# Performance work log

Measured on AMD Instinct MI355X. Metric: run time of the kernel, lower is better.

The kernel has to match this reference:

```python
import jax, jax.numpy as jnp
import numpy as np
import math

BS, SL, NE, NH = 4, 2048, 1024, 16
HD = NE // NH  # 64


def setup_inputs() -> dict:
    key = jax.random.key(0)
    ks = jax.random.split(key, 5)
    x = jax.random.normal(ks[0], (BS, SL, NE), dtype=jnp.float32)
    # causal mask: 1 where attending allowed (j <= i), 0 otherwise
    mask = jnp.tril(jnp.ones((SL, SL), dtype=jnp.int32))[None, None, :, :]
    s = 1.0 / math.sqrt(NE)
    Wqkv = jax.random.normal(ks[1], (NE, 3 * NE), dtype=jnp.float32) * s
    bqkv = jax.random.normal(ks[2], (3 * NE,), dtype=jnp.float32) * 0.02
    Wo = jax.random.normal(ks[3], (NE, NE), dtype=jnp.float32) * s
    bo = jax.random.normal(ks[4], (NE,), dtype=jnp.float32) * 0.02
    return {"x": x, "mask": mask, "Wqkv": Wqkv, "bqkv": bqkv, "Wo": Wo, "bo": bo}


def reference(x, mask, Wqkv, bqkv, Wo, bo):
    bs, sl, ne = x.shape
    qkv = x @ Wqkv + bqkv                       # [bs, sl, 3*ne]
    q, k, v = jnp.split(qkv, 3, axis=-1)
    # [bs, sl, ne] -> [bs, nh, sl, hd]
    q = q.reshape(bs, sl, NH, HD).transpose(0, 2, 1, 3)
    k = k.reshape(bs, sl, NH, HD).transpose(0, 2, 1, 3)
    v = v.reshape(bs, sl, NH, HD).transpose(0, 2, 1, 3)
    scale = 1.0 / math.sqrt(HD)
    att = jnp.einsum('bhqd,bhkd->bhqk', q, k) * scale  # [bs, nh, sl, sl]
    att = jnp.where(mask == 0, -jnp.inf, att)
    w = jax.nn.softmax(att, axis=-1)
    y = jnp.einsum('bhqk,bhkd->bhqd', w, v)            # [bs, nh, sl, hd]
    y = y.transpose(0, 2, 1, 3).reshape(bs, sl, ne)
    return y @ Wo + bo
```

## Files before the change

### kernel.cpp

```cpp
#include <hip/hip_runtime.h>

#define BS 4
#define SL 2048
#define NE 1024
#define NH 16
#define HD 64
#define N3 3072

typedef __attribute__((ext_vector_type(8))) __bf16 bf16x8;
typedef __attribute__((ext_vector_type(4))) float f32x4;
typedef __attribute__((ext_vector_type(4))) short s16x4;
typedef unsigned short u16;

#define CE 0.18033688011112042f

#if __has_builtin(__builtin_amdgcn_exp2f)
#define EXP2(x) __builtin_amdgcn_exp2f(x)
#else
#define EXP2(x) exp2f(x)
#endif

__device__ __forceinline__ u16 f2bf(float f) {
  union { float f; unsigned int u; } v; v.f = f;
  unsigned int r = v.u + 0x7FFFu + ((v.u >> 16) & 1u);
  return (u16)(r >> 16);
}

__device__ __forceinline__ int permpack(float a, float b) {
  return __builtin_amdgcn_perm(__float_as_uint(b), __float_as_uint(a),
                               0x07060302u);
}

__device__ __forceinline__ void gld16(const void* g, void* l) {
#if __has_builtin(__builtin_amdgcn_global_load_lds)
  __builtin_amdgcn_global_load_lds(
      (const __attribute__((address_space(1))) unsigned int*)g,
      (__attribute__((address_space(3))) unsigned int*)l, 16, 0, 0);
#else
  *(int4*)((char*)l + (size_t)(threadIdx.x & 63) * 16) = *(const int4*)g;
#endif
}

__global__ void convert_x(const float* __restrict__ x, u16* __restrict__ xb) {
  int i = (blockIdx.x * 256 + threadIdx.x) * 8;
  float4 f0 = *(const float4*)(x + i);
  float4 f1 = *(const float4*)(x + i + 4);
  union { int4 v; u16 h[8]; } p;
  p.h[0] = f2bf(f0.x); p.h[1] = f2bf(f0.y);
  p.h[2] = f2bf(f0.z); p.h[3] = f2bf(f0.w);
  p.h[4] = f2bf(f1.x); p.h[5] = f2bf(f1.y);
  p.h[6] = f2bf(f1.z); p.h[7] = f2bf(f1.w);
  *(int4*)(xb + i) = p.v;
}

__global__ void transpose_w(const float* __restrict__ W, u16* __restrict__ Wt,
                            int K, int N) {
  __shared__ u16 tile[32][33];
  int bn = blockIdx.x * 32, bk = blockIdx.y * 32;
  int tx = threadIdx.x, ty = threadIdx.y;
  for (int r = 0; r < 32; r += 8)
    tile[ty + r][tx] = f2bf(W[(size_t)(bk + ty + r) * N + bn + tx]);
  __syncthreads();
  for (int r = 0; r < 32; r += 8)
    Wt[(size_t)(bn + ty + r) * K + bk + tx] = tile[tx][ty + r];
}

#define MFMA_G(a, b, c) \
  __builtin_amdgcn_mfma_f32_16x16x32_bf16(a, b, c, 0, 0, 0)

template <int C32, int SCALEQ>
__global__ __launch_bounds__(256, 2) void gemm2b(
    const u16* __restrict__ A, const u16* __restrict__ Bt,
    const float* __restrict__ bias, void* __restrict__ C, int M, int N, int K,
    int lda) {
  constexpr int BM = 128, BN = 128, BK = 64;
  __shared__ u16 As[2][BM * BK];
  __shared__ u16 Bs[2][BN * BK];

  const int tid = threadIdx.x;
  const int w = tid >> 6, lane = tid & 63;
  const int lq = lane >> 4, lr = lane & 15;
  const int nwx = gridDim.x;
  const int nwg = nwx * gridDim.y;
  const int lin = blockIdx.y * nwx + blockIdx.x;
  const int cpx = nwg >> 3;
  const int swb = (lin & 7) * cpx + (lin >> 3);
  const int m0 = (swb / nwx) * BM, n0 = (swb % nwx) * BN;
  const int wm = (w >> 1) * 64, wn = (w & 1) * 64;

  const int l8 = lane >> 3, lb = lane & 7;
  const int sw8 = (lb ^ l8) * 8;
  const u16* gA = A + (size_t)(m0 + w * 32 + l8) * lda + sw8;
  const u16* gB = Bt + (size_t)(n0 + w * 32 + l8) * K + sw8;

#define STAGE(buf, gpa, gpb)                                  \
  do {                                                        \
    _Pragma("unroll") for (int c = 0; c < 4; c++) {           \
      gld16((gpa) + (size_t)(c * 8) * lda,                    \
            &As[buf][(w * 32 + c * 8) * 64]);                 \
      gld16((gpb) + (size_t)(c * 8) * K,                      \
            &Bs[buf][(w * 32 + c * 8) * 64]);                 \
    }                                                         \
  } while (0)

  const f32x4 fzero = {0.f, 0.f, 0.f, 0.f};
  f32x4 acc[4][4];
#pragma unroll
  for (int i = 0; i < 4; i++)
#pragma unroll
    for (int j = 0; j < 4; j++) acc[i][j] = fzero;

  const int KT = K / BK;
  STAGE(0, gA, gB);
  __syncthreads();
  const u16* gAn = gA + BK;
  const u16* gBn = gB + BK;

  for (int T = 0; T < KT; T++) {
    const int cur = T & 1;
    if (T + 1 < KT) {
      STAGE(cur ^ 1, gAn, gBn);
      gAn += BK;
      gBn += BK;
    }
    __builtin_amdgcn_sched_barrier(0);

    bf16x8 a[4][2], bfr[4][2];
#pragma unroll
    for (int i = 0; i < 4; i++)
#pragma unroll
      for (int ks = 0; ks < 2; ks++) {
        int row = wm + i * 16 + lr;
        a[i][ks] = *(const bf16x8*)
            &As[cur][row * 64 + (((ks * 4 + lq) ^ (lr & 7)) * 8)];
      }
#pragma unroll
    for (int j = 0; j < 4; j++)
#pragma unroll
      for (int ks = 0; ks < 2; ks++) {
        int row = wn + j * 16 + lr;
        bfr[j][ks] = *(const bf16x8*)
            &Bs[cur][row * 64 + (((ks * 4 + lq) ^ (lr & 7)) * 8)];
      }
    __builtin_amdgcn_s_setprio(1);
#pragma unroll
    for (int ks = 0; ks < 2; ks++)
#pragma unroll
      for (int i = 0; i < 4; i++)
#pragma unroll
        for (int j = 0; j < 4; j++)
          acc[i][j] = MFMA_G(a[i][ks], bfr[j][ks], acc[i][j]);
    __builtin_amdgcn_s_setprio(0);
    __syncthreads();
  }
#undef STAGE

#pragma unroll
  for (int j = 0; j < 4; j++) {
    int col = n0 + wn + j * 16 + lr;
    float bv = bias[col];
    float qs = (SCALEQ && col < NE) ? CE : 1.0f;
#pragma unroll
    for (int i = 0; i < 4; i++) {
#pragma unroll
      for (int r = 0; r < 4; r++) {
        int row = m0 + wm + i * 16 + lq * 4 + r;
        float val = acc[i][j][r] + bv;
        if (SCALEQ) val *= qs;
        if (C32) ((float*)C)[(size_t)row * N + col] = val;
        else     ((u16*)C)[(size_t)row * N + col]   = f2bf(val);
      }
    }
  }
}

#define KSTR 72
#define MFMA16(a, b, c) __builtin_amdgcn_mfma_f32_16x16x32_bf16(a, b, c, 0, 0, 0)
#define MFMA1616(a, b, c) \
  __builtin_amdgcn_mfma_f32_16x16x16bf16_1k(a, b, c, 0, 0, 0)

__device__ __forceinline__ void softmax_pack(f32x4 (&s)[4], s16x4 (&pa)[4],
                                             f32x4 (&o)[4], float& m_,
                                             float& l_) {
  float a0 = fmaxf(fmaxf(s[0][0], s[0][1]), s[0][2]);
  float a1 = fmaxf(fmaxf(s[0][3], s[1][0]), s[1][1]);
  float a2 = fmaxf(fmaxf(s[1][2], s[1][3]), s[2][0]);
  float a3 = fmaxf(fmaxf(s[2][1], s[2][2]), s[2][3]);
  float a4 = fmaxf(fmaxf(s[3][0], s[3][1]), s[3][2]);
  float mt = fmaxf(fmaxf(fmaxf(a0, a1), fmaxf(a2, a3)), fmaxf(a4, s[3][3]));
  mt = fmaxf(mt, __shfl_xor(mt, 16));
  mt = fmaxf(mt, __shfl_xor(mt, 32));
  bool need = !__all(mt <= m_ + 11.54f);
  float mn = need ? fmaxf(m_, mt) : m_;
  if (need) {
    float alpha = EXP2(m_ - mn);
    m_ = mn;
    l_ *= alpha;
#pragma unroll
    for (int jd = 0; jd < 4; jd++)
#pragma unroll
      for (int r = 0; r < 4; r++) o[jd][r] *= alpha;
  }
  float psum = 0.f;
#pragma unroll
  for (int j = 0; j < 4; j++) {
    float p0 = EXP2(s[j][0] - mn);
    float p1 = EXP2(s[j][1] - mn);
    float p2 = EXP2(s[j][2] - mn);
    float p3 = EXP2(s[j][3] - mn);
    psum += (p0 + p1) + (p2 + p3);
    union { int i[2]; s16x4 v; } pu;
    pu.i[0] = permpack(p0, p1);
    pu.i[1] = permpack(p2, p3);
    pa[j] = pu.v;
  }
  l_ += psum;
}

__device__ __forceinline__ void attn_step(const bf16x8& q0, const bf16x8& q1,
                                          const u16* __restrict__ Kb,
                                          const u16* __restrict__ Vb,
                                          bool diag, int qloc, int lq, int lr,
                                          f32x4 (&o)[4], float& m_, float& l_) {
  const f32x4 fzero = {0.f, 0.f, 0.f, 0.f};
  const int swz = (lq ^ ((lr >> 1) & 3)) * 8;
  f32x4 s[4];
  __builtin_amdgcn_s_setprio(1);
#pragma unroll
  for (int j = 0; j < 4; j++) {
    int kr = j * 16 + lr;
    bf16x8 kf0 = *(const bf16x8*)&Kb[kr * 32 + swz];
    bf16x8 kf1 = *(const bf16x8*)&Kb[2048 + kr * 32 + swz];
    f32x4 z = MFMA16(kf0, q0, fzero);
    s[j] = MFMA16(kf1, q1, z);
  }
  __builtin_amdgcn_s_setprio(0);
  if (diag) {
#pragma unroll
    for (int j = 0; j < 4; j++)
#pragma unroll
      for (int r = 0; r < 4; r++)
        if (16 * j + r > qloc) s[j][r] = -1e30f;
  }
  s16x4 pa[4];
  softmax_pack(s, pa, o, m_, l_);
  __builtin_amdgcn_s_setprio(1);
#pragma unroll
  for (int jd = 0; jd < 4; jd++) {
    const u16* vrow = &Vb[(jd * 16 + lr) * KSTR + lq * 16];
    union { int4 q; s16x4 h[2]; } va, vb;
    va.q = *(const int4*)vrow;
    vb.q = *(const int4*)(vrow + 8);
    o[jd] = MFMA1616(va.h[0], pa[0], o[jd]);
    o[jd] = MFMA1616(va.h[1], pa[1], o[jd]);
    o[jd] = MFMA1616(vb.h[0], pa[2], o[jd]);
    o[jd] = MFMA1616(vb.h[1], pa[3], o[jd]);
  }
  __builtin_amdgcn_s_setprio(0);
}

__global__ __launch_bounds__(256, 4) void attn_paired(u16* __restrict__ qkv) {
  __shared__ u16 Ks[2][4096];
  __shared__ u16 Vs[2][64 * KSTR];

  const int tid = threadIdx.x;
  const int w = tid >> 6, lane = tid & 63;
  const int lq = lane >> 4, lr = lane & 15;
  const int bh = blockIdx.x, p = blockIdx.y;
  const int h = bh & (NH - 1), b = bh >> 4;
  const int qt0 = p, qt1 = (SL / 64 - 1) - p;
  const int qloc = w * 16 + lr - 4 * lq;

  u16* base = qkv + (size_t)b * SL * N3;
  const u16* kbase = base + NE + h * HD;

  const int kg_key = lane >> 2;
  const int kg_blk = (lane & 3) ^ ((kg_key >> 1) & 3);
  const int skey = tid & 63, sd0 = (tid >> 6) * 8;
  const int skeyP = ((skey >> 2) & 3) * 16 + (skey >> 4) * 4 + (skey & 3);
  const u16* vrow0 = base + (size_t)skey * N3 + 2 * NE + h * HD + sd0;

#define KPRE(buf, key0)                                                     \
  {                                                                         \
    _Pragma("unroll") for (int t = 0; t < 2; t++) {                         \
      int chunk = w * 2 + t, half = chunk >> 2, kgrp = chunk & 3;           \
      const u16* g = kbase + (size_t)((key0) + kgrp * 16 + kg_key) * N3 +   \
                     half * 32 + kg_blk * 8;                                \
      gld16(g, &Ks[buf][half * 2048 + kgrp * 512]);                         \
    }                                                                       \
  }
#define VWRITE(buf)                                           \
  {                                                           \
    union { int4 v; u16 u[8]; } t0, t1;                       \
    t0.v = v0; t1.v = v1;                                     \
    u16* Vn = &Vs[buf][0];                                    \
    _Pragma("unroll") for (int j = 0; j < 8; j++) {           \
      Vn[(sd0 + j) * KSTR + skeyP] = t0.u[j];                 \
      Vn[(sd0 + 32 + j) * KSTR + skeyP] = t1.u[j];            \
    }                                                         \
  }

  bf16x8 qf[2][2];
#pragma unroll
  for (int half = 0; half < 2; half++) {
    int qt = half ? qt1 : qt0;
    const u16* qrow = base + (size_t)(qt * 64 + w * 16 + lr) * N3 + h * HD;
    qf[half][0] = *(const bf16x8*)(qrow + lq * 8);
    qf[half][1] = *(const bf16x8*)(qrow + 32 + lq * 8);
  }

  const f32x4 fzero = {0.f, 0.f, 0.f, 0.f};
  f32x4 o[2][4];
  float m_[2], l_[2];
#pragma unroll
  for (int half = 0; half < 2; half++) {
    m_[half] = -1e30f;
    l_[half] = 0.f;
#pragma unroll
    for (int jd = 0; jd < 4; jd++) o[half][jd] = fzero;
  }

  KPRE(0, 0);
  int4 v0 = *(const int4*)vrow0;
  int4 v1 = *(const int4*)(vrow0 + 32);
  asm volatile("s_waitcnt vmcnt(0)" ::: "memory");
  VWRITE(0);
  {
    const u16* nv = vrow0 + (size_t)64 * N3;
    v0 = *(const int4*)nv;
    v1 = *(const int4*)(nv + 32);
  }

  const int ktend = qt1 + 1;
  for (int kt = 0; kt < ktend; kt++) {
    __syncthreads();
    const int nb = (kt + 1) & 1;
    if (kt + 1 < ktend) {
      KPRE(nb, (kt + 1) * 64);
      VWRITE(nb);
      if (kt + 2 < ktend) {
        const u16* nv = vrow0 + (size_t)(kt + 2) * 64 * N3;
        v0 = *(const int4*)nv;
        v1 = *(const int4*)(nv + 32);
      }
    }
    __builtin_amdgcn_sched_barrier(0);

    const u16* Kb = &Ks[kt & 1][0];
    const u16* Vb = &Vs[kt & 1][0];
    attn_step(qf[1][0], qf[1][1], Kb, Vb, kt == qt1, qloc, lq, lr, o[1], m_[1],
              l_[1]);
    if (kt <= qt0)
      attn_step(qf[0][0], qf[0][1], Kb, Vb, kt == qt0, qloc, lq, lr, o[0],
                m_[0], l_[0]);
  }

#pragma unroll
  for (int half = 0; half < 2; half++) {
    int qt = half ? qt1 : qt0;
    float lsum = l_[half];
    lsum += __shfl_xor(lsum, 16);
    lsum += __shfl_xor(lsum, 32);
    float inv = 1.0f / lsum;
    u16* yrow = base + (size_t)(qt * 64 + w * 16 + lr) * N3 + h * HD;
#pragma unroll
    for (int jd = 0; jd < 4; jd++) {
      int2 val;
      val.x = (int)(((unsigned)f2bf(o[half][jd][1] * inv) << 16) |
                    f2bf(o[half][jd][0] * inv));
      val.y = (int)(((unsigned)f2bf(o[half][jd][3] * inv) << 16) |
                    f2bf(o[half][jd][2] * inv));
      *(int2*)(yrow + 16 * jd + 4 * lq) = val;
    }
  }
}

extern "C" void kernel_launch(void* const* d_in, const int* in_sizes, int n_in,
                              void* d_out, int out_size, void* d_ws,
                              size_t ws_size, hipStream_t stream) {
  const float* x    = (const float*)d_in[0];
  const float* Wqkv = (const float*)d_in[2];
  const float* bqkv = (const float*)d_in[3];
  const float* Wo   = (const float*)d_in[4];
  const float* bo   = (const float*)d_in[5];

  u16* WqkvT  = (u16*)d_ws;
  u16* WoT    = WqkvT + (size_t)N3 * NE;
  u16* xb     = WoT + (size_t)NE * NE;
  u16* qkvbuf = xb + (size_t)BS * SL * NE;

  convert_x<<<(BS * SL * NE) / (256 * 8), 256, 0, stream>>>(x, xb);
  transpose_w<<<dim3(N3 / 32, NE / 32), dim3(32, 8), 0, stream>>>(Wqkv, WqkvT,
                                                                  NE, N3);
  transpose_w<<<dim3(NE / 32, NE / 32), dim3(32, 8), 0, stream>>>(Wo, WoT, NE,
                                                                  NE);
  gemm2b<0, 1><<<dim3(N3 / 128, (BS * SL) / 128), 256, 0, stream>>>(
      xb, WqkvT, bqkv, qkvbuf, BS * SL, N3, NE, NE);
  attn_paired<<<dim3(BS * NH, SL / 128), 256, 0, stream>>>(qkvbuf);
  gemm2b<1, 0><<<dim3(NE / 128, (BS * SL) / 128), 256, 0, stream>>>(
      qkvbuf, WoT, bo, d_out, BS * SL, NE, NE, N3);
}
```

Before: 261.8 us.

## Triple-buffer GEMM with BK=32 and pack V transpose writes as dwords

The GEMM moves from a double-buffered BK=64 pipeline to a triple-buffered BK=32 one, with explicit vmcnt waits and raw barriers so two stages of loads stay in flight. Occupancy is raised to three workgroups per CU. The attention V staging now loads two adjacent keys per thread and uses byte-perm to write 32-bit pairs into the transposed LDS tile, replacing 16-bit scattered stores. This trades more barriers per K (the k-loop has twice as many iterations) for deeper prefetch and fewer LDS store instructions.

```diff
diff --git a/kernel.cpp b/kernel.cpp
--- a/kernel.cpp
+++ b/kernel.cpp
@@ -39,6 +39,14 @@
 #else
   *(int4*)((char*)l + (size_t)(threadIdx.x & 63) * 16) = *(const int4*)g;
 #endif
+}
+
+template <int N>
+__device__ __forceinline__ void vmw() {
+  if constexpr (N == 0)
+    asm volatile("s_waitcnt vmcnt(0)" ::: "memory");
+  else if constexpr (N == 4)
+    asm volatile("s_waitcnt vmcnt(4)" ::: "memory");
 }
 
 __global__ void convert_x(const float* __restrict__ x, u16* __restrict__ xb) {
@@ -67,15 +75,21 @@
 
 #define MFMA_G(a, b, c) \
   __builtin_amdgcn_mfma_f32_16x16x32_bf16(a, b, c, 0, 0, 0)
+#define GBAR()                         \
+  do {                                 \
+    __builtin_amdgcn_s_barrier();      \
+    __builtin_amdgcn_sched_barrier(0); \
+  } while (0)
 
 template <int C32, int SCALEQ>
-__global__ __launch_bounds__(256, 2) void gemm2b(
+__global__ __launch_bounds__(256, 3) void gemm3b(
     const u16* __restrict__ A, const u16* __restrict__ Bt,
     const float* __restrict__ bias, void* __restrict__ C, int M, int N, int K,
     int lda) {
-  constexpr int BM = 128, BN = 128, BK = 64;
-  __shared__ u16 As[2][BM * BK];
-  __shared__ u16 Bs[2][BN * BK];
+  constexpr int BM = 128, BN = 128, BK = 32;
+  constexpr int TSZ = BM * BK;
+  __shared__ u16 As[3][TSZ];
+  __shared__ u16 Bs[3][TSZ];
 
   const int tid = threadIdx.x;
   const int w = tid >> 6, lane = tid & 63;
@@ -88,18 +102,18 @@
   const int m0 = (swb / nwx) * BM, n0 = (swb % nwx) * BN;
   const int wm = (w >> 1) * 64, wn = (w & 1) * 64;
 
-  const int l8 = lane >> 3, lb = lane & 7;
-  const int sw8 = (lb ^ l8) * 8;
-  const u16* gA = A + (size_t)(m0 + w * 32 + l8) * lda + sw8;
-  const u16* gB = Bt + (size_t)(n0 + w * 32 + l8) * K + sw8;
-
-#define STAGE(buf, gpa, gpb)                                  \
+  const int srow = lane >> 2;
+  const int swcol = ((lane & 3) ^ ((lane >> 3) & 3)) * 8;
+  const u16* gA = A + (size_t)(m0 + w * 32 + srow) * lda + swcol;
+  const u16* gB = Bt + (size_t)(n0 + w * 32 + srow) * K + swcol;
+
+#define STAGE3(abuf, bbuf, gpa, gpb)                          \
   do {                                                        \
-    _Pragma("unroll") for (int c = 0; c < 4; c++) {           \
-      gld16((gpa) + (size_t)(c * 8) * lda,                    \
-            &As[buf][(w * 32 + c * 8) * 64]);                 \
-      gld16((gpb) + (size_t)(c * 8) * K,                      \
-            &Bs[buf][(w * 32 + c * 8) * 64]);                 \
+    _Pragma("unroll") for (int c = 0; c < 2; c++) {           \
+      gld16((gpa) + (size_t)(c * 16) * lda,                   \
+            (abuf) + (w * 32 + c * 16) * 32);                 \
+      gld16((gpb) + (size_t)(c * 16) * K,                     \
+            (bbuf) + (w * 32 + c * 16) * 32);                 \
     }                                                         \
   } while (0)
 
@@ -111,49 +125,53 @@
     for (int j = 0; j < 4; j++) acc[i][j] = fzero;
 
   const int KT = K / BK;
-  STAGE(0, gA, gB);
-  __syncthreads();
-  const u16* gAn = gA + BK;
-  const u16* gBn = gB + BK;
-
+  u16* asb = &As[0][0];
+  u16* bsb = &Bs[0][0];
+  STAGE3(asb, bsb, gA, gB);
+  STAGE3(asb + TSZ, bsb + TSZ, gA + BK, gB + BK);
+  vmw<4>();
+  GBAR();
+  const u16* gAn = gA + 2 * BK;
+  const u16* gBn = gB + 2 * BK;
+
+  int cur = 0, stg = 2;
+  const int fswz = (lq ^ ((lr >> 1) & 3)) * 8;
   for (int T = 0; T < KT; T++) {
-    const int cur = T & 1;
-    if (T + 1 < KT) {
-      STAGE(cur ^ 1, gAn, gBn);
+    if (T + 2 < KT) {
+      STAGE3(asb + stg * TSZ, bsb + stg * TSZ, gAn, gBn);
       gAn += BK;
       gBn += BK;
     }
     __builtin_amdgcn_sched_barrier(0);
 
-    bf16x8 a[4][2], bfr[4][2];
+    const u16* Ac = asb + cur * TSZ;
+    const u16* Bc = bsb + cur * TSZ;
+    bf16x8 a[4], b[4];
 #pragma unroll
     for (int i = 0; i < 4; i++)
-#pragma unroll
-      for (int ks = 0; ks < 2; ks++) {
-        int row = wm + i * 16 + lr;
-        a[i][ks] = *(const bf16x8*)
-            &As[cur][row * 64 + (((ks * 4 + lq) ^ (lr & 7)) * 8)];
-      }
+      a[i] = *(const bf16x8*)&Ac[(wm + i * 16 + lr) * 32 + fswz];
 #pragma unroll
     for (int j = 0; j < 4; j++)
-#pragma unroll
-      for (int ks = 0; ks < 2; ks++) {
-        int row = wn + j * 16 + lr;
-        bfr[j][ks] = *(const bf16x8*)
-            &Bs[cur][row * 64 + (((ks * 4 + lq) ^ (lr & 7)) * 8)];
-      }
+      b[j] = *(const bf16x8*)&Bc[(wn + j * 16 + lr) * 32 + fswz];
     __builtin_amdgcn_s_setprio(1);
 #pragma unroll
-    for (int ks = 0; ks < 2; ks++)
-#pragma unroll
-      for (int i = 0; i < 4; i++)
-#pragma unroll
-        for (int j = 0; j < 4; j++)
-          acc[i][j] = MFMA_G(a[i][ks], bfr[j][ks], acc[i][j]);
+    for (int i = 0; i < 4; i++)
+#pragma unroll
+      for (int j = 0; j < 4; j++)
+        acc[i][j] = MFMA_G(a[i], b[j], acc[i][j]);
     __builtin_amdgcn_s_setprio(0);
-    __syncthreads();
-  }
-#undef STAGE
+
+    if (T + 2 < KT) {
+      vmw<4>();
+      GBAR();
+    } else if (T + 1 < KT) {
+      vmw<0>();
+      GBAR();
+    }
+    cur = (cur == 2) ? 0 : cur + 1;
+    stg = (stg == 2) ? 0 : stg + 1;
+  }
+#undef STAGE3
 
 #pragma unroll
   for (int j = 0; j < 4; j++) {
@@ -276,9 +294,10 @@
 
   const int kg_key = lane >> 2;
   const int kg_blk = (lane & 3) ^ ((kg_key >> 1) & 3);
-  const int skey = tid & 63, sd0 = (tid >> 6) * 8;
-  const int skeyP = ((skey >> 2) & 3) * 16 + (skey >> 4) * 4 + (skey & 3);
-  const u16* vrow0 = base + (size_t)skey * N3 + 2 * NE + h * HD + sd0;
+  const int sd0 = (tid >> 5) * 8;
+  const int k0 = (tid & 31) * 2;
+  const int k0p = ((k0 >> 2) & 3) * 16 + (k0 >> 4) * 4 + (k0 & 3);
+  const u16* vrow0 = base + (size_t)k0 * N3 + 2 * NE + h * HD + sd0;
 
 #define KPRE(buf, key0)                                                     \
   {                                                                         \
@@ -289,15 +308,19 @@
       gld16(g, &Ks[buf][half * 2048 + kgrp * 512]);                         \
     }                                                                       \
   }
-#define VWRITE(buf)                                           \
-  {                                                           \
-    union { int4 v; u16 u[8]; } t0, t1;                       \
-    t0.v = v0; t1.v = v1;                                     \
-    u16* Vn = &Vs[buf][0];                                    \
-    _Pragma("unroll") for (int j = 0; j < 8; j++) {           \
-      Vn[(sd0 + j) * KSTR + skeyP] = t0.u[j];                 \
-      Vn[(sd0 + 32 + j) * KSTR + skeyP] = t1.u[j];            \
-    }                                                         \
+#define VWRITE(buf)                                                        \
+  {                                                                        \
+    union { int4 v; int d[4]; } t0, t1;                                    \
+    t0.v = v0; t1.v = v1;                                                  \
+    u16* Vn = &Vs[buf][0];                                                 \
+    _Pragma("unroll") for (int dw = 0; dw < 4; dw++) {                     \
+      int lo = __builtin_amdgcn_perm((unsigned)t1.d[dw],                   \
+                                     (unsigned)t0.d[dw], 0x05040100u);     \
+      int hi = __builtin_amdgcn_perm((unsigned)t1.d[dw],                   \
+                                     (unsigned)t0.d[dw], 0x07060302u);     \
+      *(int*)&Vn[(sd0 + 2 * dw) * KSTR + k0p] = lo;                        \
+      *(int*)&Vn[(sd0 + 2 * dw + 1) * KSTR + k0p] = hi;                    \
+    }                                                                      \
   }
 
   bf16x8 qf[2][2];
@@ -322,13 +345,13 @@
 
   KPRE(0, 0);
   int4 v0 = *(const int4*)vrow0;
-  int4 v1 = *(const int4*)(vrow0 + 32);
+  int4 v1 = *(const int4*)(vrow0 + N3);
   asm volatile("s_waitcnt vmcnt(0)" ::: "memory");
   VWRITE(0);
   {
     const u16* nv = vrow0 + (size_t)64 * N3;
     v0 = *(const int4*)nv;
-    v1 = *(const int4*)(nv + 32);
+    v1 = *(const int4*)(nv + N3);
   }
 
   const int ktend = qt1 + 1;
@@ -341,7 +364,7 @@
       if (kt + 2 < ktend) {
         const u16* nv = vrow0 + (size_t)(kt + 2) * 64 * N3;
         v0 = *(const int4*)nv;
-        v1 = *(const int4*)(nv + 32);
+        v1 = *(const int4*)(nv + N3);
       }
     }
     __builtin_amdgcn_sched_barrier(0);
@@ -394,9 +417,9 @@
                                                                   NE, N3);
   transpose_w<<<dim3(NE / 32, NE / 32), dim3(32, 8), 0, stream>>>(Wo, WoT, NE,
                                                                   NE);
-  gemm2b<0, 1><<<dim3(N3 / 128, (BS * SL) / 128), 256, 0, stream>>>(
+  gemm3b<0, 1><<<dim3(N3 / 128, (BS * SL) / 128), 256, 0, stream>>>(
       xb, WqkvT, bqkv, qkvbuf, BS * SL, N3, NE, NE);
   attn_paired<<<dim3(BS * NH, SL / 128), 256, 0, stream>>>(qkvbuf);
-  gemm2b<1, 0><<<dim3(NE / 128, (BS * SL) / 128), 256, 0, stream>>>(
+  gemm3b<1, 0><<<dim3(NE / 128, (BS * SL) / 128), 256, 0, stream>>>(
       qkvbuf, WoT, bo, d_out, BS * SL, NE, NE, N3);
 }
```

Measured after the change: 259.8 us. About the same (-0.8%).
